# Performance work log

Hardware: AMD Instinct MI355X
Metric: run time of the kernel (lower is better)

Reference implementation:

```python
import jax, jax.numpy as jnp
import numpy as np

D_MODEL = 1024
N_HEADS = 16
HEAD_DIM = D_MODEL // N_HEADS
D_FF = 4096
B, S = 2, 2048
EPS = 1e-6
NEG = -1e9


def setup_inputs() -> dict:
    key = jax.random.key(0)
    ks = jax.random.split(key, 16)
    sd = 1.0 / np.sqrt(D_MODEL)
    sf = 1.0 / np.sqrt(D_FF)
    inp = {
        "x": jax.random.normal(ks[0], (B, S, D_MODEL), jnp.float32),
        # causal mask, broadcastable over batch and heads
        "mask": jnp.tril(jnp.ones((S, S), jnp.bool_))[None, None, :, :],
        # attention projections, torch Linear layout [out, in]
        "Wq": jax.random.normal(ks[1], (D_MODEL, D_MODEL), jnp.float32) * sd,
        "bq": jnp.zeros((D_MODEL,), jnp.float32),
        "Wk": jax.random.normal(ks[2], (D_MODEL, D_MODEL), jnp.float32) * sd,
        "bk": jnp.zeros((D_MODEL,), jnp.float32),
        "Wv": jax.random.normal(ks[3], (D_MODEL, D_MODEL), jnp.float32) * sd,
        "bv": jnp.zeros((D_MODEL,), jnp.float32),
        "Wo": jax.random.normal(ks[4], (D_MODEL, D_MODEL), jnp.float32) * sd,
        "bo": jnp.zeros((D_MODEL,), jnp.float32),
        # layer norms
        "ln1_g": jnp.ones((D_MODEL,), jnp.float32),
        "ln1_b": jnp.zeros((D_MODEL,), jnp.float32),
        "ln2_g": jnp.ones((D_MODEL,), jnp.float32),
        "ln2_b": jnp.zeros((D_MODEL,), jnp.float32),
        # FFN
        "W1": jax.random.normal(ks[5], (D_FF, D_MODEL), jnp.float32) * sd,
        "b1": jnp.zeros((D_FF,), jnp.float32),
        "W2": jax.random.normal(ks[6], (D_MODEL, D_FF), jnp.float32) * sf,
        "b2": jnp.zeros((D_MODEL,), jnp.float32),
    }
    return inp


def _layer_norm(x, g, b):
    mu = jnp.mean(x, axis=-1, keepdims=True)
    var = jnp.var(x, axis=-1, keepdims=True)
    return (x - mu) * jax.lax.rsqrt(var + EPS) * g + b


def _linear(x, W, b):
    return jnp.einsum('...i,oi->...o', x, W) + b


def _attention(x, mask, Wq, bq, Wk, bk, Wv, bv, Wo, bo):
    Bsz, Sq, _ = x.shape
    q = _linear(x, Wq, bq).reshape(Bsz, Sq, N_HEADS, HEAD_DIM)
    k = _linear(x, Wk, bk).reshape(Bsz, Sq, N_HEADS, HEAD_DIM)
    v = _linear(x, Wv, bv).reshape(Bsz, Sq, N_HEADS, HEAD_DIM)
    # [B,H,S,S]
    scores = jnp.einsum('bqhd,bkhd->bhqk', q, k) / np.sqrt(HEAD_DIM)
    scores = jnp.where(mask, scores, NEG)
    weights = jax.nn.softmax(scores, axis=-1)
    ctx = jnp.einsum('bhqk,bkhd->bqhd', weights, v).reshape(Bsz, Sq, D_MODEL)
    return _linear(ctx, Wo, bo)


def reference(x, mask, Wq, bq, Wk, bk, Wv, bv, Wo, bo,
              ln1_g, ln1_b, ln2_g, ln2_b, W1, b1, W2, b2):
    # pre-LN attention block (dropout = identity at inference)
    h = _layer_norm(x, ln1_g, ln1_b)
    x = x + _attention(h, mask, Wq, bq, Wk, bk, Wv, bv, Wo, bo)
    # pre-LN FFN block
    h = _layer_norm(x, ln2_g, ln2_b)
    h = jax.nn.gelu(_linear(h, W1, b1), approximate=False)
    x = x + _linear(h, W2, b2)
    return x
```

## Files before the change

kernel.cpp:

```cpp
#include <hip/hip_runtime.h>
#include <hip/hip_bf16.h>
#include <cstdint>
#include <cstddef>

typedef unsigned short u16;
typedef __bf16 bf16x8 __attribute__((ext_vector_type(8)));
typedef float f32x4 __attribute__((ext_vector_type(4)));

#define D_MODEL 1024
#define D_FF    4096
#define BATCH   2
#define SEQ     2048
#define NH      16
#define HD      64
#define ROWS    (BATCH*SEQ)
#define QKVS    3072

__device__ __forceinline__ u16 f2bf(float f) {
    union { float f; uint32_t u; } v; v.f = f;
    uint32_t u = v.u;
    u += 0x7FFF + ((u >> 16) & 1);
    return (u16)(u >> 16);
}

__device__ __forceinline__ uint32_t cvtpk_bf16(float lo, float hi) {
    uint32_t r;
    asm("v_cvt_pk_bf16_f32 %0, %1, %2" : "=v"(r) : "v"(lo), "v"(hi));
    return r;
}

__device__ __forceinline__ bf16x8 ldg8(const u16* p) {
    return *reinterpret_cast<const bf16x8*>(p);
}

__device__ __forceinline__ f32x4 mfma16(bf16x8 a, bf16x8 b, f32x4 c) {
    return __builtin_amdgcn_mfma_f32_16x16x32_bf16(a, b, c, 0, 0, 0);
}

__device__ __forceinline__ void gld_lds16(const void* g, void* l) {
    __builtin_amdgcn_global_load_lds(
        (const __attribute__((address_space(1))) void*)g,
        (__attribute__((address_space(3))) void*)l, 16, 0, 0);
}

__device__ __forceinline__ float gelu_f(float x) {
    float u = fmaf(0.044715f * x, x * x, x);
    float z = fminf(-2.3022036f * u, 126.0f);
    float e = __builtin_amdgcn_exp2f(z);
    return x / (1.0f + e);
}

struct alignas(8) U16x4 { u16 x, y, z, w; };

__global__ void cvt_all(const float* __restrict__ s0, const float* __restrict__ s1,
                        const float* __restrict__ s2, const float* __restrict__ s3,
                        const float* __restrict__ s4, const float* __restrict__ s5,
                        u16* __restrict__ out)
{
    const size_t MM1 = 1 << 20;
    size_t i = ((size_t)blockIdx.x * 256 + threadIdx.x) * 4;
    const float* src; size_t off;
    if      (i <     MM1) { src = s0; off = i; }
    else if (i < 2 * MM1) { src = s1; off = i - MM1; }
    else if (i < 3 * MM1) { src = s2; off = i - 2 * MM1; }
    else if (i < 4 * MM1) { src = s3; off = i - 3 * MM1; }
    else if (i < 8 * MM1) { src = s4; off = i - 4 * MM1; }
    else                  { src = s5; off = i - 8 * MM1; }
    float4 f = *reinterpret_cast<const float4*>(src + off);
    U16x4 o{ f2bf(f.x), f2bf(f.y), f2bf(f.z), f2bf(f.w) };
    *reinterpret_cast<U16x4*>(out + i) = o;
}

__global__ __launch_bounds__(256) void ln_bf16(
    const float* __restrict__ x, const float* __restrict__ g,
    const float* __restrict__ b, u16* __restrict__ out)
{
    int row = blockIdx.x;
    const float* xr = x + (size_t)row * D_MODEL;
    int t = threadIdx.x;
    float4 v = *reinterpret_cast<const float4*>(xr + t * 4);
    float s = v.x + v.y + v.z + v.w;
    float q = v.x*v.x + v.y*v.y + v.z*v.z + v.w*v.w;
    #pragma unroll
    for (int off = 1; off < 64; off <<= 1) {
        s += __shfl_xor(s, off);
        q += __shfl_xor(q, off);
    }
    __shared__ float red[8];
    if ((t & 63) == 0) { red[(t >> 6) * 2] = s; red[(t >> 6) * 2 + 1] = q; }
    __syncthreads();
    float sum = red[0] + red[2] + red[4] + red[6];
    float sq  = red[1] + red[3] + red[5] + red[7];
    float mu  = sum * (1.0f / D_MODEL);
    float var = sq * (1.0f / D_MODEL) - mu * mu;
    float rstd = rsqrtf(var + 1e-6f);
    float4 gg = *reinterpret_cast<const float4*>(g + t * 4);
    float4 bb = *reinterpret_cast<const float4*>(b + t * 4);
    U16x4 o{ f2bf((v.x - mu) * rstd * gg.x + bb.x),
             f2bf((v.y - mu) * rstd * gg.y + bb.y),
             f2bf((v.z - mu) * rstd * gg.z + bb.z),
             f2bf((v.w - mu) * rstd * gg.w + bb.w) };
    *reinterpret_cast<U16x4*>(out + (size_t)row * D_MODEL + t * 4) = o;
}

#define EPI_BF16   0
#define EPI_RESF32 1
#define EPI_GELU   2
#define EPI_PART   3

template<int EPI>
__global__ __launch_bounds__(256, 4) void gemm97(
    const u16* __restrict__ A, const u16* __restrict__ B,
    const float* __restrict__ bias, const float* __restrict__ res,
    u16* __restrict__ outb, float* __restrict__ outf,
    int M, int N, int K, int KS)
{
    __shared__ u16 As[128 * 64];
    __shared__ u16 Bs[128 * 64];
    const int t = threadIdx.x;
    const int lane = t & 63, w = t >> 6;
    const int lr = lane & 15, lg = lane >> 4;
    const int wrr = (w >> 1) * 64, wcc = (w & 1) * 64;
    const int brow = blockIdx.y * 128, bcol = blockIdx.x * 128;
    const u16* Ag = A + (size_t)brow * KS;
    const u16* Bg = B + (size_t)bcol * KS;

    f32x4 acc[4][4] = {};
    const int NT = K >> 6;

    for (int kt = 0; kt < NT; ++kt) {
        #pragma unroll
        for (int c = 0; c < 4; ++c) {
            int f = c * 256 + t;
            int row = f >> 3, slot = f & 7;
            int sg = slot ^ (row & 7);
            gld_lds16(Ag + (size_t)row * KS + kt * 64 + sg * 8, As + f * 8);
            gld_lds16(Bg + (size_t)row * KS + kt * 64 + sg * 8, Bs + f * 8);
        }
        __syncthreads();

        bf16x8 af[4][2];
        #pragma unroll
        for (int mi = 0; mi < 4; ++mi) {
            int row = wrr + mi * 16 + lr;
            const u16* bp = As + row * 64;
            int key = row & 7;
            af[mi][0] = ldg8(bp + ((0 + lg) ^ key) * 8);
            af[mi][1] = ldg8(bp + ((4 + lg) ^ key) * 8);
        }
        __builtin_amdgcn_s_setprio(1);
        #pragma unroll
        for (int ni = 0; ni < 4; ++ni) {
            int row = wcc + ni * 16 + lr;
            const u16* bp = Bs + row * 64;
            int key = row & 7;
            bf16x8 b0 = ldg8(bp + ((0 + lg) ^ key) * 8);
            bf16x8 b1 = ldg8(bp + ((4 + lg) ^ key) * 8);
            #pragma unroll
            for (int mi = 0; mi < 4; ++mi) {
                acc[mi][ni] = mfma16(af[mi][0], b0, acc[mi][ni]);
                acc[mi][ni] = mfma16(af[mi][1], b1, acc[mi][ni]);
            }
        }
        __builtin_amdgcn_s_setprio(0);
        __syncthreads();
    }

    #pragma unroll
    for (int mi = 0; mi < 4; ++mi) {
        int r0 = brow + wrr + mi * 16 + lg * 4;
        #pragma unroll
        for (int ni = 0; ni < 4; ++ni) {
            int c = bcol + wcc + ni * 16 + lr;
            float bv = bias[c];
            #pragma unroll
            for (int j = 0; j < 4; ++j) {
                float v = acc[mi][ni][j] + bv;
                size_t idx = (size_t)(r0 + j) * N + c;
                if constexpr (EPI == EPI_GELU) {
                    outb[idx] = f2bf(gelu_f(v));
                } else if constexpr (EPI == EPI_RESF32) {
                    outf[idx] = v + res[idx];
                } else {
                    outb[idx] = f2bf(v);
                }
            }
        }
    }
}

template<int EPI>
__global__ __launch_bounds__(256, 2) void gemm_bt(
    const u16* __restrict__ A, const u16* __restrict__ B,
    const float* __restrict__ bias, const float* __restrict__ res,
    u16* __restrict__ outb, float* __restrict__ outf,
    int M, int N, int K, int KS)
{
    __shared__ u16 As[2][128 * 64];
    __shared__ u16 Bs[2][128 * 64];
    const int t = threadIdx.x;
    const int lane = t & 63;
    const int w = t >> 6;
    const int lr = lane & 15, lg = lane >> 4;
    const int wrr = (w >> 1) * 64, wcc = (w & 1) * 64;
    const int brow = blockIdx.y * 128, bcol = blockIdx.x * 128;
    const int kz = blockIdx.z;
    const u16* Ag = A + (size_t)brow * KS + (size_t)kz * K;
    const u16* Bg = B + (size_t)bcol * KS + (size_t)kz * K;

    f32x4 acc[4][4] = {};

    const int NT = K >> 6;

    auto stage = [&](int buf, int kt) {
        const u16* ga = Ag + kt * 64;
        const u16* gb = Bg + kt * 64;
        u16* la = As[buf];
        u16* lb = Bs[buf];
        #pragma unroll
        for (int c = 0; c < 4; ++c) {
            int f = c * 256 + t;
            int row = f >> 3, slot = f & 7;
            int sg = slot ^ (row & 7);
            gld_lds16(ga + (size_t)row * KS + sg * 8, la + f * 8);
            gld_lds16(gb + (size_t)row * KS + sg * 8, lb + f * 8);
        }
    };

    auto compute = [&](int buf) {
        const u16* la = As[buf];
        const u16* lb = Bs[buf];
        bf16x8 af[4][2];
        #pragma unroll
        for (int mi = 0; mi < 4; ++mi) {
            int row = wrr + mi * 16 + lr;
            int base = row * 64;
            af[mi][0] = *reinterpret_cast<const bf16x8*>(la + base + ((0 + lg) ^ (row & 7)) * 8);
            af[mi][1] = *reinterpret_cast<const bf16x8*>(la + base + ((4 + lg) ^ (row & 7)) * 8);
        }
        __builtin_amdgcn_s_setprio(1);
        #pragma unroll
        for (int ni = 0; ni < 4; ++ni) {
            int row = wcc + ni * 16 + lr;
            int base = row * 64;
            bf16x8 b0 = *reinterpret_cast<const bf16x8*>(lb + base + ((0 + lg) ^ (row & 7)) * 8);
            bf16x8 b1 = *reinterpret_cast<const bf16x8*>(lb + base + ((4 + lg) ^ (row & 7)) * 8);
            #pragma unroll
            for (int mi = 0; mi < 4; ++mi) {
                acc[mi][ni] = mfma16(af[mi][0], b0, acc[mi][ni]);
                acc[mi][ni] = mfma16(af[mi][1], b1, acc[mi][ni]);
            }
        }
        __builtin_amdgcn_s_setprio(0);
    };

    stage(0, 0);
    if (NT > 1) {
        stage(1, 1);
        asm volatile("s_waitcnt vmcnt(8)" ::: "memory");
    } else {
        asm volatile("s_waitcnt vmcnt(0)" ::: "memory");
    }
    __builtin_amdgcn_s_barrier();

    for (int kt = 0; kt < NT; ++kt) {
        compute(kt & 1);
        if (kt + 1 == NT) break;
        __builtin_amdgcn_s_barrier();
        if (kt + 2 < NT) {
            stage(kt & 1, kt + 2);
            asm volatile("s_waitcnt vmcnt(8)" ::: "memory");
        } else {
            asm volatile("s_waitcnt vmcnt(0)" ::: "memory");
        }
        __builtin_amdgcn_s_barrier();
    }

    #pragma unroll
    for (int mi = 0; mi < 4; ++mi) {
        int r0 = brow + wrr + mi * 16 + lg * 4;
        #pragma unroll
        for (int ni = 0; ni < 4; ++ni) {
            int c = bcol + wcc + ni * 16 + lr;
            float bv = 0.f;
            if constexpr (EPI != EPI_PART) bv = bias[c];
            #pragma unroll
            for (int j = 0; j < 4; ++j) {
                float v = acc[mi][ni][j] + bv;
                size_t idx = (size_t)(r0 + j) * N + c;
                if constexpr (EPI == EPI_GELU) {
                    outb[idx] = f2bf(gelu_f(v));
                } else if constexpr (EPI == EPI_RESF32) {
                    outf[idx] = v + res[idx];
                } else if constexpr (EPI == EPI_PART) {
                    outf[idx + (size_t)kz * M * N] = v;
                } else {
                    outb[idx] = f2bf(v);
                }
            }
        }
    }
}

__global__ void ffn2_reduce(const float* __restrict__ p,
                            const float* __restrict__ b2,
                            const float* __restrict__ x2,
                            float* __restrict__ out)
{
    size_t i = ((size_t)blockIdx.x * 256 + threadIdx.x) * 4;
    float4 a0 = *reinterpret_cast<const float4*>(p + i);
    float4 a1 = *reinterpret_cast<const float4*>(p + (size_t)ROWS * D_MODEL + i);
    float4 r  = *reinterpret_cast<const float4*>(x2 + i);
    float4 bb = *reinterpret_cast<const float4*>(b2 + (i & (D_MODEL - 1)));
    float4 o;
    o.x = a0.x + a1.x + r.x + bb.x;
    o.y = a0.y + a1.y + r.y + bb.y;
    o.z = a0.z + a1.z + r.z + bb.z;
    o.w = a0.w + a1.w + r.w + bb.w;
    *reinterpret_cast<float4*>(out + i) = o;
}

__global__ __launch_bounds__(256) void vtrans(
    const u16* __restrict__ QKV, u16* __restrict__ VT)
{
    __shared__ u16 tile[64][72];
    const int st = blockIdx.x * 64;
    const int bh = blockIdx.y;
    const int b = bh >> 4, h = bh & 15;
    const int t = threadIdx.x;

    #pragma unroll
    for (int c = 0; c < 2; ++c) {
        int tok = c * 32 + (t >> 3);
        int d0 = (t & 7) * 8;
        bf16x8 v = ldg8(QKV + ((size_t)(b * SEQ + st + tok)) * QKVS + 2048 + h * HD + d0);
        *reinterpret_cast<bf16x8*>(&tile[tok][d0]) = v;
    }
    __syncthreads();
    u16* dst = VT + (size_t)bh * HD * SEQ + st;
    #pragma unroll
    for (int c = 0; c < 2; ++c) {
        int d = c * 32 + (t >> 3);
        int tok0 = (t & 7) * 8;
        u16 vals[8];
        #pragma unroll
        for (int i = 0; i < 8; ++i) vals[i] = tile[tok0 + i][d];
        *reinterpret_cast<bf16x8*>(dst + (size_t)d * SEQ + tok0) =
            *reinterpret_cast<const bf16x8*>(vals);
    }
}

#define QBLK  64
#define KVBLK 64

__global__ __launch_bounds__(256, 3) void attn7(
    const u16* __restrict__ QKV, const u16* __restrict__ VT,
    u16* __restrict__ O)
{
    __shared__ u16 Ks[2][64 * 64];
    __shared__ u16 Vs[2][64 * 64];
    __shared__ u16 Pl[4][16 * 72];

    const int i  = blockIdx.x;
    const int bh = blockIdx.y;
    const int b = bh >> 4, h = bh & 15;
    const int qta = 31 - i;
    const int qtb = i;
    const int q0a = qta * QBLK, q0b = qtb * QBLK;
    const int t = threadIdx.x;
    const int lane = t & 63, w = t >> 6;
    const int lr = lane & 15, lg = lane >> 4;

    const size_t rowbase = (size_t)b * SEQ;
    const u16* Qg = QKV + rowbase * QKVS + h * HD;
    const u16* Kg = Qg + 1024;
    const u16* Vg = VT + (size_t)bh * HD * SEQ;

    const u16* qpa = Qg + (size_t)(q0a + w * 16 + lr) * QKVS;
    const u16* qpb = Qg + (size_t)(q0b + w * 16 + lr) * QKVS;
    bf16x8 qa0 = ldg8(qpa + lg * 8), qa1 = ldg8(qpa + 32 + lg * 8);
    bf16x8 qb0 = ldg8(qpb + lg * 8), qb1 = ldg8(qpb + 32 + lg * 8);

    f32x4 oa[4] = {}, ob[4] = {};
    float lsa[4] = {}, lsb[4] = {};

    const int ntiles = qta + 1;
    u16* Pw = Pl[w];
    const float SC = 0.125f * 1.44269504089f;

    auto stage = [&](int buf, int tt) {
        const int kv0 = tt * KVBLK;
        #pragma unroll
        for (int c = 0; c < 2; ++c) {
            int f = c * 256 + t;
            int row = f >> 3, slot = f & 7;
            int sgk = slot ^ ((row >> 2) & 7);
            int sgv = slot ^ (row & 7);
            gld_lds16(Kg + (size_t)(kv0 + row) * QKVS + sgk * 8, Ks[buf] + f * 8);
            gld_lds16(Vg + (size_t)row * SEQ + kv0 + sgv * 8, Vs[buf] + f * 8);
        }
    };

    auto qtile = [&](bf16x8 qf0, bf16x8 qf1, f32x4* o, float* ls,
                     int q0, int kv0, bool diag, const u16* kb, const u16* vb) {
        f32x4 s[4] = {};
        __builtin_amdgcn_s_setprio(1);
        #pragma unroll
        for (int ni = 0; ni < 4; ++ni) {
            int row = lr * 4 + ni;
            const u16* base = kb + row * 64;
            int key = (row >> 2) & 7;
            bf16x8 k0 = *reinterpret_cast<const bf16x8*>(base + ((0 + lg) ^ key) * 8);
            bf16x8 k1 = *reinterpret_cast<const bf16x8*>(base + ((4 + lg) ^ key) * 8);
            s[ni] = mfma16(qf0, k0, s[ni]);
            s[ni] = mfma16(qf1, k1, s[ni]);
        }
        __builtin_amdgcn_s_setprio(0);

        #pragma unroll
        for (int j = 0; j < 4; ++j) {
            int qi = q0 + w * 16 + lg * 4 + j;
            float p0 = __builtin_amdgcn_exp2f(s[0][j] * SC);
            float p1 = __builtin_amdgcn_exp2f(s[1][j] * SC);
            float p2 = __builtin_amdgcn_exp2f(s[2][j] * SC);
            float p3 = __builtin_amdgcn_exp2f(s[3][j] * SC);
            if (diag) {
                int kvb = kv0 + lr * 4;
                p0 = (kvb     <= qi) ? p0 : 0.f;
                p1 = (kvb + 1 <= qi) ? p1 : 0.f;
                p2 = (kvb + 2 <= qi) ? p2 : 0.f;
                p3 = (kvb + 3 <= qi) ? p3 : 0.f;
            }
            ls[j] += (p0 + p1) + (p2 + p3);
            uint2 pk = make_uint2(cvtpk_bf16(p0, p1), cvtpk_bf16(p2, p3));
            *reinterpret_cast<uint2*>(&Pw[(lg * 4 + j) * 72 + lr * 4]) = pk;
        }

        bf16x8 pa0 = *reinterpret_cast<const bf16x8*>(Pw + lr * 72 + lg * 8);
        bf16x8 pa1 = *reinterpret_cast<const bf16x8*>(Pw + lr * 72 + 32 + lg * 8);
        __builtin_amdgcn_s_setprio(1);
        #pragma unroll
        for (int ni = 0; ni < 4; ++ni) {
            int row = ni * 16 + lr;
            const u16* base = vb + row * 64;
            bf16x8 v0 = *reinterpret_cast<const bf16x8*>(base + ((0 + lg) ^ (row & 7)) * 8);
            bf16x8 v1 = *reinterpret_cast<const bf16x8*>(base + ((4 + lg) ^ (row & 7)) * 8);
            o[ni] = mfma16(pa0, v0, o[ni]);
            o[ni] = mfma16(pa1, v1, o[ni]);
        }
        __builtin_amdgcn_s_setprio(0);
    };

    stage(0, 0);
    stage(1, 1);
    asm volatile("s_waitcnt vmcnt(4)" ::: "memory");
    __builtin_amdgcn_s_barrier();

    for (int tt = 0; tt < ntiles; ++tt) {
        const int buf = tt & 1;
        const int kv0 = tt * KVBLK;
        const u16* kb = Ks[buf];
        const u16* vb = Vs[buf];

        qtile(qa0, qa1, oa, lsa, q0a, kv0, tt == qta, kb, vb);
        if (tt <= qtb)
            qtile(qb0, qb1, ob, lsb, q0b, kv0, tt == qtb, kb, vb);

        if (tt + 1 == ntiles) break;
        __builtin_amdgcn_s_barrier();
        if (tt + 2 < ntiles) {
            stage(buf, tt + 2);
            asm volatile("s_waitcnt vmcnt(4)" ::: "memory");
        } else {
            asm volatile("s_waitcnt vmcnt(0)" ::: "memory");
        }
        __builtin_amdgcn_s_barrier();
    }

    #pragma unroll
    for (int j = 0; j < 4; ++j) {
        float va = lsa[j], vb2 = lsb[j];
        va += __shfl_xor(va, 1); vb2 += __shfl_xor(vb2, 1);
        va += __shfl_xor(va, 2); vb2 += __shfl_xor(vb2, 2);
        va += __shfl_xor(va, 4); vb2 += __shfl_xor(vb2, 4);
        va += __shfl_xor(va, 8); vb2 += __shfl_xor(vb2, 8);
        lsa[j] = va; lsb[j] = vb2;
    }

    u16* Oa = O + (rowbase + q0a + w * 16) * D_MODEL + h * HD;
    u16* Ob = O + (rowbase + q0b + w * 16) * D_MODEL + h * HD;
    #pragma unroll
    for (int j = 0; j < 4; ++j) {
        float inva = 1.0f / lsa[j];
        float invb = 1.0f / lsb[j];
        int r = (lg * 4 + j) * D_MODEL;
        #pragma unroll
        for (int ni = 0; ni < 4; ++ni) {
            Oa[r + ni * 16 + lr] = f2bf(oa[ni][j] * inva);
            Ob[r + ni * 16 + lr] = f2bf(ob[ni][j] * invb);
        }
    }
}

extern "C" void kernel_launch(void* const* d_in, const int* in_sizes, int n_in,
                              void* d_out, int out_size, void* d_ws, size_t ws_size,
                              hipStream_t stream)
{
    (void)in_sizes; (void)n_in; (void)out_size; (void)ws_size;
    const float* x   = (const float*)d_in[0];
    const float* Wq  = (const float*)d_in[2];
    const float* bq  = (const float*)d_in[3];
    const float* Wk  = (const float*)d_in[4];
    const float* bk  = (const float*)d_in[5];
    const float* Wv  = (const float*)d_in[6];
    const float* bv  = (const float*)d_in[7];
    const float* Wo  = (const float*)d_in[8];
    const float* bo  = (const float*)d_in[9];
    const float* g1  = (const float*)d_in[10];
    const float* be1 = (const float*)d_in[11];
    const float* g2  = (const float*)d_in[12];
    const float* be2 = (const float*)d_in[13];
    const float* W1  = (const float*)d_in[14];
    const float* b1  = (const float*)d_in[15];
    const float* W2  = (const float*)d_in[16];
    const float* b2  = (const float*)d_in[17];
    float* out = (float*)d_out;

    const size_t MM = 1 << 20;
    u16* Wqkv_b = (u16*)d_ws;
    u16* Wo_b = Wqkv_b + 3 * MM;
    u16* W1_b = Wo_b + MM;
    u16* W2_b = W1_b + 4 * MM;
    u16* hbuf = W2_b + 4 * MM;
    u16* QKVb = hbuf + 4 * MM;
    u16* ctx  = QKVb + 12 * MM;
    u16* ffn1 = ctx + 4 * MM;
    float* x2 = (float*)(ffn1 + 16 * MM);
    float* bqkv = (float*)(x2 + 4 * MM);
    u16* VTb = hbuf;
    float* fpart = (float*)QKVb;

    cvt_all<<<12 * MM / 1024, 256, 0, stream>>>(Wq, Wk, Wv, Wo, W1, W2, Wqkv_b);

    hipMemcpyAsync(bqkv,        bq, D_MODEL * sizeof(float), hipMemcpyDeviceToDevice, stream);
    hipMemcpyAsync(bqkv + 1024, bk, D_MODEL * sizeof(float), hipMemcpyDeviceToDevice, stream);
    hipMemcpyAsync(bqkv + 2048, bv, D_MODEL * sizeof(float), hipMemcpyDeviceToDevice, stream);

    ln_bf16<<<ROWS, 256, 0, stream>>>(x, g1, be1, hbuf);

    dim3 gqkv(QKVS / 128, ROWS / 128);
    gemm97<EPI_BF16><<<gqkv, 256, 0, stream>>>(hbuf, Wqkv_b, bqkv, nullptr,
                                               QKVb, nullptr, ROWS, QKVS, 1024, 1024);

    vtrans<<<dim3(SEQ / 64, BATCH * NH), 256, 0, stream>>>(QKVb, VTb);

    dim3 ga(SEQ / QBLK / 2, BATCH * NH);
    attn7<<<ga, 256, 0, stream>>>(QKVb, VTb, ctx);

    dim3 gq(D_MODEL / 128, ROWS / 128);
    gemm_bt<EPI_RESF32><<<gq, 256, 0, stream>>>(ctx, Wo_b, bo, x, nullptr, x2,
                                                ROWS, D_MODEL, 1024, 1024);

    ln_bf16<<<ROWS, 256, 0, stream>>>(x2, g2, be2, hbuf);

    dim3 gf1(D_FF / 128, ROWS / 128);
    gemm97<EPI_GELU><<<gf1, 256, 0, stream>>>(hbuf, W1_b, b1, nullptr, ffn1, nullptr,
                                              ROWS, D_FF, 1024, 1024);

    dim3 gf2(D_MODEL / 128, ROWS / 128, 2);
    gemm_bt<EPI_PART><<<gf2, 256, 0, stream>>>(ffn1, W2_b, nullptr, nullptr,
                                               nullptr, fpart, ROWS, D_MODEL, 2048, 4096);
    ffn2_reduce<<<(ROWS * D_MODEL) / 1024, 256, 0, stream>>>(fpart, b2, x2, out);
}
```

Baseline: 238.0 us.

## Triple-buffer K in attention with split K/V staging; swap GEMM grid order

The attention kernel now stages K and V separately, with K triple-buffered and V double-buffered. Each iteration issues the next V and the K two tiles ahead under a single barrier, where the old loop used two barriers. The goal is deeper prefetch and less barrier stall. Separately, the QKV, W1 and Wo GEMM grids swap blockIdx.x/y so that consecutive blocks walk along M rather than N, which changes L2 reuse of the weight tiles. The new vmcnt accounting adds a risk of races if the counts are wrong.

```diff
diff --git a/kernel.cpp b/kernel.cpp
--- a/kernel.cpp
+++ b/kernel.cpp
@@ -121,7 +121,7 @@
     const int lane = t & 63, w = t >> 6;
     const int lr = lane & 15, lg = lane >> 4;
     const int wrr = (w >> 1) * 64, wcc = (w & 1) * 64;
-    const int brow = blockIdx.y * 128, bcol = blockIdx.x * 128;
+    const int brow = blockIdx.x * 128, bcol = blockIdx.y * 128;
     const u16* Ag = A + (size_t)brow * KS;
     const u16* Bg = B + (size_t)bcol * KS;
 
@@ -189,7 +189,7 @@
     }
 }
 
-template<int EPI>
+template<int EPI, int RM>
 __global__ __launch_bounds__(256, 2) void gemm_bt(
     const u16* __restrict__ A, const u16* __restrict__ B,
     const float* __restrict__ bias, const float* __restrict__ res,
@@ -203,7 +203,8 @@
     const int w = t >> 6;
     const int lr = lane & 15, lg = lane >> 4;
     const int wrr = (w >> 1) * 64, wcc = (w & 1) * 64;
-    const int brow = blockIdx.y * 128, bcol = blockIdx.x * 128;
+    const int brow = (RM ? blockIdx.x : blockIdx.y) * 128;
+    const int bcol = (RM ? blockIdx.y : blockIdx.x) * 128;
     const int kz = blockIdx.z;
     const u16* Ag = A + (size_t)brow * KS + (size_t)kz * K;
     const u16* Bg = B + (size_t)bcol * KS + (size_t)kz * K;
@@ -353,11 +354,11 @@
 #define QBLK  64
 #define KVBLK 64
 
-__global__ __launch_bounds__(256, 3) void attn7(
+__global__ __launch_bounds__(256, 3) void attn8(
     const u16* __restrict__ QKV, const u16* __restrict__ VT,
     u16* __restrict__ O)
 {
-    __shared__ u16 Ks[2][64 * 64];
+    __shared__ u16 Ks[3][64 * 64];
     __shared__ u16 Vs[2][64 * 64];
     __shared__ u16 Pl[4][16 * 72];
 
@@ -388,15 +389,23 @@
     u16* Pw = Pl[w];
     const float SC = 0.125f * 1.44269504089f;
 
-    auto stage = [&](int buf, int tt) {
+    auto stageK = [&](int buf, int tt) {
         const int kv0 = tt * KVBLK;
         #pragma unroll
         for (int c = 0; c < 2; ++c) {
             int f = c * 256 + t;
             int row = f >> 3, slot = f & 7;
             int sgk = slot ^ ((row >> 2) & 7);
+            gld_lds16(Kg + (size_t)(kv0 + row) * QKVS + sgk * 8, Ks[buf] + f * 8);
+        }
+    };
+    auto stageV = [&](int buf, int tt) {
+        const int kv0 = tt * KVBLK;
+        #pragma unroll
+        for (int c = 0; c < 2; ++c) {
+            int f = c * 256 + t;
+            int row = f >> 3, slot = f & 7;
             int sgv = slot ^ (row & 7);
-            gld_lds16(Kg + (size_t)(kv0 + row) * QKVS + sgk * 8, Ks[buf] + f * 8);
             gld_lds16(Vg + (size_t)row * SEQ + kv0 + sgv * 8, Vs[buf] + f * 8);
         }
     };
@@ -451,30 +460,28 @@
         __builtin_amdgcn_s_setprio(0);
     };
 
-    stage(0, 0);
-    stage(1, 1);
-    asm volatile("s_waitcnt vmcnt(4)" ::: "memory");
-    __builtin_amdgcn_s_barrier();
+    stageV(0, 0);
+    stageK(0, 0);
+    stageK(1, 1);
 
     for (int tt = 0; tt < ntiles; ++tt) {
-        const int buf = tt & 1;
+        __builtin_amdgcn_s_barrier();
+        if (tt + 1 < ntiles) stageV((tt + 1) & 1, tt + 1);
+        if (tt + 2 < ntiles) stageK((tt + 2) % 3, tt + 2);
+        if (tt + 2 < ntiles)
+            asm volatile("s_waitcnt vmcnt(6)" ::: "memory");
+        else if (tt + 1 < ntiles)
+            asm volatile("s_waitcnt vmcnt(4)" ::: "memory");
+        else
+            asm volatile("s_waitcnt vmcnt(0)" ::: "memory");
+
         const int kv0 = tt * KVBLK;
-        const u16* kb = Ks[buf];
-        const u16* vb = Vs[buf];
+        const u16* kb = Ks[tt % 3];
+        const u16* vb = Vs[tt & 1];
 
         qtile(qa0, qa1, oa, lsa, q0a, kv0, tt == qta, kb, vb);
         if (tt <= qtb)
             qtile(qb0, qb1, ob, lsb, q0b, kv0, tt == qtb, kb, vb);
-
-        if (tt + 1 == ntiles) break;
-        __builtin_amdgcn_s_barrier();
-        if (tt + 2 < ntiles) {
-            stage(buf, tt + 2);
-            asm volatile("s_waitcnt vmcnt(4)" ::: "memory");
-        } else {
-            asm volatile("s_waitcnt vmcnt(0)" ::: "memory");
-        }
-        __builtin_amdgcn_s_barrier();
     }
 
     #pragma unroll
@@ -548,27 +555,27 @@
 
     ln_bf16<<<ROWS, 256, 0, stream>>>(x, g1, be1, hbuf);
 
-    dim3 gqkv(QKVS / 128, ROWS / 128);
+    dim3 gqkv(ROWS / 128, QKVS / 128);
     gemm97<EPI_BF16><<<gqkv, 256, 0, stream>>>(hbuf, Wqkv_b, bqkv, nullptr,
                                                QKVb, nullptr, ROWS, QKVS, 1024, 1024);
 
     vtrans<<<dim3(SEQ / 64, BATCH * NH), 256, 0, stream>>>(QKVb, VTb);
 
     dim3 ga(SEQ / QBLK / 2, BATCH * NH);
-    attn7<<<ga, 256, 0, stream>>>(QKVb, VTb, ctx);
-
-    dim3 gq(D_MODEL / 128, ROWS / 128);
-    gemm_bt<EPI_RESF32><<<gq, 256, 0, stream>>>(ctx, Wo_b, bo, x, nullptr, x2,
-                                                ROWS, D_MODEL, 1024, 1024);
+    attn8<<<ga, 256, 0, stream>>>(QKVb, VTb, ctx);
+
+    dim3 gq(ROWS / 128, D_MODEL / 128);
+    gemm_bt<EPI_RESF32, 1><<<gq, 256, 0, stream>>>(ctx, Wo_b, bo, x, nullptr, x2,
+                                                   ROWS, D_MODEL, 1024, 1024);
 
     ln_bf16<<<ROWS, 256, 0, stream>>>(x2, g2, be2, hbuf);
 
-    dim3 gf1(D_FF / 128, ROWS / 128);
+    dim3 gf1(ROWS / 128, D_FF / 128);
     gemm97<EPI_GELU><<<gf1, 256, 0, stream>>>(hbuf, W1_b, b1, nullptr, ffn1, nullptr,
                                               ROWS, D_FF, 1024, 1024);
 
     dim3 gf2(D_MODEL / 128, ROWS / 128, 2);
-    gemm_bt<EPI_PART><<<gf2, 256, 0, stream>>>(ffn1, W2_b, nullptr, nullptr,
-                                               nullptr, fpart, ROWS, D_MODEL, 2048, 4096);
+    gemm_bt<EPI_PART, 0><<<gf2, 256, 0, stream>>>(ffn1, W2_b, nullptr, nullptr,
+                                                  nullptr, fpart, ROWS, D_MODEL, 2048, 4096);
     ffn2_reduce<<<(ROWS * D_MODEL) / 1024, 256, 0, stream>>>(fpart, b2, x2, out);
 }
```

Result: faster. 233.1 us (-2.0%).
